# Optimization experiments

Measured on AMD Instinct MI355X. Metric: run time of the kernel, lower is better.

## Reference

```python
import jax, jax.numpy as jnp
import numpy as np

B, N, P = 8, 4096, 1024
P4 = P // 4
EPS = 1e-5


def _ln(x, g, b):
    mu = jnp.mean(x, axis=-1, keepdims=True)
    var = jnp.var(x, axis=-1, keepdims=True)
    return (x - mu) * jax.lax.rsqrt(var + EPS) * g + b


def setup_inputs() -> dict:
    key = jax.random.key(0)
    ks = jax.random.split(key, 16)
    s = lambda fan: 1.0 / np.sqrt(fan)
    return {
        "xyz": jax.random.normal(ks[0], (B, N, 3), jnp.float32),
        "x": jax.random.normal(ks[1], (B, N, P), jnp.float32),
        "ln1_g": jnp.ones((P,), jnp.float32),
        "ln1_b": jnp.zeros((P,), jnp.float32),
        "ln2_g": jnp.ones((P,), jnp.float32),
        "ln2_b": jnp.zeros((P,), jnp.float32),
        "qk_w": jax.random.normal(ks[2], (P4, P), jnp.float32) * s(P),   # shared q/k 1x1 conv, no bias
        "v_w": jax.random.normal(ks[3], (P, P), jnp.float32) * s(P),
        "v_b": jax.random.normal(ks[4], (P,), jnp.float32) * s(P),
        "t1_w": jax.random.normal(ks[5], (P, P4), jnp.float32) * s(P4),  # trans_conv
        "t1_b": jax.random.normal(ks[6], (P,), jnp.float32) * s(P4),
        "t2_w": jax.random.normal(ks[7], (P, P4), jnp.float32) * s(P4),  # trans_conv1
        "t2_b": jax.random.normal(ks[8], (P,), jnp.float32) * s(P4),
        "m1_w": jax.random.normal(ks[9], (P, P), jnp.float32) * s(P),
        "m1_b": jax.random.normal(ks[10], (P,), jnp.float32) * s(P),
        "m2_w": jax.random.normal(ks[11], (P, P), jnp.float32) * s(P),
        "m2_b": jax.random.normal(ks[12], (P,), jnp.float32) * s(P),
    }


def reference(xyz, x, ln1_g, ln1_b, ln2_g, ln2_b, qk_w, v_w, v_b,
              t1_w, t1_b, t2_w, t2_b, m1_w, m1_b, m2_w, m2_b):
    # xyz is accepted but unused, matching the torch module. Dropout = eval identity.
    res1 = x
    h = _ln(x, ln1_g, ln1_b)                                   # [B,N,P]
    # TransformerBlock_1 (1x1 convs on h^T [B,P,N] are just matmuls over P)
    x_q = jnp.einsum('op,bnp->bon', qk_w, h)                   # [B,P4,N]
    # k shares weights with q; x_k permuted is x_q transposed
    x_v = jnp.einsum('op,bnp->bno', v_w, h) + v_b              # [B,N,P]
    energy = jnp.einsum('bqn,bkn->bqk', x_q, x_q)              # [B,P4,P4]
    att = jnp.einsum('op,bpk->bok', t1_w, energy) + t1_b[:, None]   # [B,P,P4]
    att = jax.nn.gelu(att, approximate=False)
    att = jnp.einsum('op,bkp->bok', t2_w, att) + t2_b[:, None]      # [B,P,P]
    att = jax.nn.softmax(att, axis=-1)
    t_out = jnp.einsum('bnp,bpq->bnq', x_v, att)               # [B,N,P]
    x1 = t_out + res1
    h2 = _ln(x1, ln2_g, ln2_b)
    m = jax.nn.gelu(h2 @ m1_w.T + m1_b, approximate=False)
    m = m @ m2_w.T + m2_b
    return x1 + m
```

## Files before the change

### kernel.cpp

```cpp
#include <hip/hip_runtime.h>


typedef __attribute__((ext_vector_type(4))) float f32x4;
typedef __attribute__((ext_vector_type(8))) _Float16 h16x8;
typedef __attribute__((ext_vector_type(8))) unsigned short u16x8;
typedef __attribute__((ext_vector_type(4))) unsigned short u16x4;

__device__ __forceinline__ unsigned short f2h(float f) {
  _Float16 h = (_Float16)f;
  return __builtin_bit_cast(unsigned short, h);
}
__device__ __forceinline__ float h2f(unsigned short u) {
  return (float)__builtin_bit_cast(_Float16, u);
}
__device__ __forceinline__ unsigned split16(float f) {
  _Float16 h = (_Float16)f;
  _Float16 l = (_Float16)(f - (float)h);
  return (unsigned)__builtin_bit_cast(unsigned short, h) |
         ((unsigned)__builtin_bit_cast(unsigned short, l) << 16);
}
__device__ __forceinline__ float gelu_f(float x) {
  return 0.5f * x * (1.0f + erff(x * 0.70710678118654752f));
}
__device__ __forceinline__ void gload16(const void* g, void* l) {
  __builtin_amdgcn_global_load_lds(
      (const __attribute__((address_space(1))) unsigned int*)g,
      (__attribute__((address_space(3))) unsigned int*)l, 16, 0, 0);
}
#define FENCE() asm volatile("" ::: "memory")

__device__ __forceinline__ void xcd_swz(int& bx, int& by, int gx, int gy) {
  const int nwg = gx * gy;
  if ((nwg & 7) == 0 && nwg >= 16) {
    const int flat = bx + gx * by;
    const int chunk = nwg >> 3;
    const int nf = (flat & 7) * chunk + (flat >> 3);
    bx = nf % gx;
    by = nf / gx;
  }
}

__global__ __launch_bounds__(256)
void lnsplit_kernel(const float* __restrict__ x, unsigned short* __restrict__ xhi,
                    float* __restrict__ muis) {
  __shared__ float red[16];
  const size_t base = (size_t)blockIdx.x * 1024;
  const int t = threadIdx.x;
  f32x4 v = *(const f32x4*)&x[base + t * 4];
  float s = v[0] + v[1] + v[2] + v[3];
  float q = v[0] * v[0] + v[1] * v[1] + v[2] * v[2] + v[3] * v[3];
#pragma unroll
  for (int o = 32; o > 0; o >>= 1) { s += __shfl_down(s, o); q += __shfl_down(q, o); }
  const int w = t >> 6;
  if ((t & 63) == 0) { red[w] = s; red[8 + w] = q; }
  u16x4 oh;
#pragma unroll
  for (int j = 0; j < 4; j++) oh[j] = f2h(v[j]);
  *(u16x4*)&xhi[base + t * 4] = oh;
  __syncthreads();
  if (t == 0) {
    s = (red[0] + red[1]) + (red[2] + red[3]);
    q = (red[8] + red[9]) + (red[10] + red[11]);
    const float mu = s * (1.0f / 1024.0f);
    const float var = q * (1.0f / 1024.0f) - mu * mu;
    muis[blockIdx.x * 2] = mu;
    muis[blockIdx.x * 2 + 1] = rsqrtf(var + 1e-5f);
  }
}

__global__ __launch_bounds__(256)
void stats16_kernel(const unsigned short* __restrict__ x16, float* __restrict__ muis) {
  __shared__ float red[16];
  const size_t base = (size_t)blockIdx.x * 1024;
  const int t = threadIdx.x;
  u16x4 raw = *(const u16x4*)&x16[base + t * 4];
  float v[4];
#pragma unroll
  for (int j = 0; j < 4; j++) v[j] = h2f(raw[j]);
  float s = v[0] + v[1] + v[2] + v[3];
  float q = v[0] * v[0] + v[1] * v[1] + v[2] * v[2] + v[3] * v[3];
#pragma unroll
  for (int o = 32; o > 0; o >>= 1) { s += __shfl_down(s, o); q += __shfl_down(q, o); }
  const int w = t >> 6;
  if ((t & 63) == 0) { red[w] = s; red[8 + w] = q; }
  __syncthreads();
  if (t == 0) {
    s = (red[0] + red[1]) + (red[2] + red[3]);
    q = (red[8] + red[9]) + (red[10] + red[11]);
    const float mu = s * (1.0f / 1024.0f);
    const float var = q * (1.0f / 1024.0f) - mu * mu;
    muis[blockIdx.x * 2] = mu;
    muis[blockIdx.x * 2 + 1] = rsqrtf(var + 1e-5f);
  }
}

__global__ __launch_bounds__(256)
void cvt_kernel(const float* __restrict__ in, unsigned short* __restrict__ hi,
                unsigned short* __restrict__ lo, int n4) {
  int i = blockIdx.x * 256 + threadIdx.x;
  if (i < n4) {
    f32x4 v = *(const f32x4*)&in[(size_t)i * 4];
    u16x4 oh, ol;
#pragma unroll
    for (int j = 0; j < 4; j++) {
      unsigned p = split16(v[j]);
      oh[j] = (unsigned short)(p & 0xffffu);
      ol[j] = (unsigned short)(p >> 16);
    }
    *(u16x4*)&hi[(size_t)i * 4] = oh;
    if (lo) *(u16x4*)&lo[(size_t)i * 4] = ol;
  }
}

__global__ __launch_bounds__(256)
void wqprep_kernel(const float* __restrict__ qkw, const float* __restrict__ lng,
                   const float* __restrict__ lnb, unsigned short* __restrict__ wh,
                   unsigned short* __restrict__ wl, float* __restrict__ S,
                   float* __restrict__ B0) {
  __shared__ float red[16];
  const int o = blockIdx.x;
  const int t = threadIdx.x;
  const float* row = qkw + (size_t)o * 1024;
  f32x4 wv = *(const f32x4*)&row[t * 4];
  f32x4 gv = *(const f32x4*)&lng[t * 4];
  f32x4 bv = *(const f32x4*)&lnb[t * 4];
  float s = 0.0f, d = 0.0f;
  u16x4 oh, ol;
#pragma unroll
  for (int j = 0; j < 4; j++) {
    float wg = wv[j] * gv[j];
    unsigned p = split16(wg);
    oh[j] = (unsigned short)(p & 0xffffu);
    ol[j] = (unsigned short)(p >> 16);
    s += wg;
    d += wv[j] * bv[j];
  }
  *(u16x4*)&wh[(size_t)o * 1024 + t * 4] = oh;
  *(u16x4*)&wl[(size_t)o * 1024 + t * 4] = ol;
#pragma unroll
  for (int off = 32; off > 0; off >>= 1) { s += __shfl_down(s, off); d += __shfl_down(d, off); }
  const int w = t >> 6;
  if ((t & 63) == 0) { red[w] = s; red[8 + w] = d; }
  __syncthreads();
  if (t == 0) {
    S[o] = (red[0] + red[1]) + (red[2] + red[3]);
    B0[o] = (red[8] + red[9]) + (red[10] + red[11]);
  }
}

__global__ __launch_bounds__(256)
void m1prep_kernel(const float* __restrict__ m1w, const float* __restrict__ lng,
                   const float* __restrict__ lnb, const float* __restrict__ m1b,
                   unsigned short* __restrict__ wp, float* __restrict__ S,
                   float* __restrict__ b2) {
  __shared__ float red[16];
  const int o = blockIdx.x;
  const int t = threadIdx.x;
  const float* row = m1w + (size_t)o * 1024;
  f32x4 wv = *(const f32x4*)&row[t * 4];
  f32x4 gv = *(const f32x4*)&lng[t * 4];
  f32x4 bv = *(const f32x4*)&lnb[t * 4];
  float s = 0.0f, d = 0.0f;
  u16x4 ow;
#pragma unroll
  for (int j = 0; j < 4; j++) {
    float wpj = wv[j] * gv[j];
    ow[j] = f2h(wpj);
    s += wpj;
    d += wv[j] * bv[j];
  }
  *(u16x4*)&wp[(size_t)o * 1024 + t * 4] = ow;
#pragma unroll
  for (int off = 32; off > 0; off >>= 1) { s += __shfl_down(s, off); d += __shfl_down(d, off); }
  const int w = t >> 6;
  if ((t & 63) == 0) { red[w] = s; red[8 + w] = d; }
  __syncthreads();
  if (t == 0) {
    S[o] = (red[0] + red[1]) + (red[2] + red[3]);
    b2[o] = m1b[o] + (red[8] + red[9]) + (red[10] + red[11]);
  }
}

__global__ __launch_bounds__(256)
void vwvec_kernel(const float* __restrict__ vw, const float* __restrict__ lng,
                  const float* __restrict__ lnb, const float* __restrict__ vb,
                  float* __restrict__ gv, float* __restrict__ vb2) {
  __shared__ float red[16];
  const int p = blockIdx.x;
  const int t = threadIdx.x;
  const float* row = vw + (size_t)p * 1024;
  f32x4 wv = *(const f32x4*)&row[t * 4];
  f32x4 gg = *(const f32x4*)&lng[t * 4];
  f32x4 bb = *(const f32x4*)&lnb[t * 4];
  float s = 0.0f, d = 0.0f;
#pragma unroll
  for (int j = 0; j < 4; j++) { s += wv[j] * gg[j]; d += wv[j] * bb[j]; }
#pragma unroll
  for (int off = 32; off > 0; off >>= 1) { s += __shfl_down(s, off); d += __shfl_down(d, off); }
  const int w = t >> 6;
  if ((t & 63) == 0) { red[w] = s; red[8 + w] = d; }
  __syncthreads();
  if (t == 0) {
    gv[p] = (red[0] + red[1]) + (red[2] + red[3]);
    vb2[p] = vb[p] + (red[8] + red[9]) + (red[10] + red[11]);
  }
}

__global__ __launch_bounds__(256)
void vwt_kernel(const float* __restrict__ vw, const float* __restrict__ lng,
                unsigned short* __restrict__ wvt) {
  __shared__ float T[64][65];
  const int bx = blockIdx.x, by = blockIdx.y;
  const int t = threadIdx.x;
  const int lr = t >> 6, lc = t & 63;
#pragma unroll
  for (int i = 0; i < 16; ++i) {
    const int row = i * 4 + lr;
    T[row][lc] = vw[(size_t)(by * 64 + row) * 1024 + bx * 64 + lc];
  }
  __syncthreads();
#pragma unroll
  for (int i = 0; i < 16; ++i) {
    const int row = i * 4 + lr;
    wvt[(size_t)(bx * 64 + row) * 1024 + by * 64 + lc] =
        f2h(T[lc][row] * lng[bx * 64 + row]);
  }
}

__global__ __launch_bounds__(256)
void attdots_kernel(const unsigned short* __restrict__ attT, const float* __restrict__ vb2,
                    const float* __restrict__ gv, float* __restrict__ add1,
                    float* __restrict__ Sg) {
  const int b = blockIdx.y;
  const int q = blockIdx.x * 4 + (threadIdx.x >> 6);
  const int l = threadIdx.x & 63;
  const unsigned short* row = attT + ((size_t)b * 1024 + q) * 1024;
  float s = 0.0f, d = 0.0f;
#pragma unroll
  for (int i = 0; i < 2; ++i) {
    u16x8 v = *(const u16x8*)&row[(i * 64 + l) * 8];
#pragma unroll
    for (int j = 0; j < 8; j++) {
      const float a = h2f(v[j]);
      const int idx = (i * 64 + l) * 8 + j;
      s += a * vb2[idx];
      d += a * gv[idx];
    }
  }
#pragma unroll
  for (int o = 32; o > 0; o >>= 1) { s += __shfl_down(s, o); d += __shfl_down(d, o); }
  if (l == 0) { add1[b * 1024 + q] = s; Sg[b * 1024 + q] = d; }
}

template <int EPI>
__global__ __launch_bounds__(256)
void gemm_v(const unsigned short* __restrict__ Ain, const unsigned short* __restrict__ Bin,
            void* __restrict__ Cout, const float* __restrict__ bias,
            const unsigned short* __restrict__ res16In, const float* __restrict__ muis,
            const float* __restrict__ Svec,
            int K, int lda, int ldb, int ldc,
            long long sA, long long sB, long long sC, long long sBias, long long sRes) {
  __shared__ short As[2][4096];
  __shared__ short Bs[2][4096];
  const int z = blockIdx.z;
  const unsigned short* A = Ain + (size_t)z * sA;
  const unsigned short* B = Bin + (size_t)z * sB;
  int bx = blockIdx.x, by = blockIdx.y;
  xcd_swz(bx, by, gridDim.x, gridDim.y);
  const int mBase = by * 128, nBase = bx * 128;
  const int t = threadIdx.x, w = t >> 6, l = t & 63;
  const int r16 = l & 15, kq = l >> 4;
  const int wr = (w >> 1) * 64, wc = (w & 1) * 64;
  f32x4 acc[4][4] = {};

  auto stage = [&](int buf, int k0) {
#pragma unroll
    for (int i = 0; i < 2; ++i) {
      const int c = i * 256 + t;
      const int row = c >> 2, cc = c & 3;
      const int gc = cc ^ ((row >> 1) & 3);
      short* la = &As[buf][(i * 256 + w * 64) * 8];
      short* lb = &Bs[buf][(i * 256 + w * 64) * 8];
      gload16(&A[(size_t)(mBase + row) * lda + k0 + gc * 8], la);
      gload16(&B[(size_t)(nBase + row) * ldb + k0 + gc * 8], lb);
    }
  };

  const int nt = K >> 5;
  stage(0, 0);
  if (nt > 1) stage(1, 32);
  for (int ts = 0; ts < nt; ++ts) {
    const int cur = ts & 1;
    if (ts + 1 < nt) { asm volatile("s_waitcnt vmcnt(4)" ::: "memory"); }
    else             { asm volatile("s_waitcnt vmcnt(0)" ::: "memory"); }
    __builtin_amdgcn_s_barrier();
    FENCE();
    h16x8 aF[4], bF[4];
#pragma unroll
    for (int mi = 0; mi < 4; mi++) {
      const int r = wr + mi * 16 + r16;
      aF[mi] = *(const h16x8*)&As[cur][r * 32 + (kq ^ ((r >> 1) & 3)) * 8];
    }
#pragma unroll
    for (int ni = 0; ni < 4; ni++) {
      const int r = wc + ni * 16 + r16;
      bF[ni] = *(const h16x8*)&Bs[cur][r * 32 + (kq ^ ((r >> 1) & 3)) * 8];
    }
    __builtin_amdgcn_s_setprio(1);
#pragma unroll
    for (int mi = 0; mi < 4; mi++)
#pragma unroll
      for (int ni = 0; ni < 4; ni++)
        acc[mi][ni] = __builtin_amdgcn_mfma_f32_16x16x32_f16(aF[mi], bF[ni], acc[mi][ni], 0, 0, 0);
    __builtin_amdgcn_s_setprio(0);
    FENCE();
    __builtin_amdgcn_s_barrier();
    FENCE();
    if (ts + 2 < nt) stage(cur, (ts + 2) * 32);
  }
  FENCE();

  unsigned short* C16 = (unsigned short*)Cout + (size_t)z * sC;
  float* C32 = (float*)Cout + (size_t)z * sC;
  const float* bp = (EPI != 4) ? bias + (size_t)z * sBias : nullptr;
  const unsigned short* rp = (EPI == 3) ? res16In + (size_t)z * sRes : nullptr;

  if constexpr (EPI == 4 || EPI == 9) {
    short* ep = ((w & 2) ? &Bs[0][0] : &As[0][0]) + (w & 1) * 4096;
#pragma unroll
    for (int mi = 0; mi < 4; mi++) {
      float mu[4], is[4];
      if (EPI == 9) {
#pragma unroll
        for (int r = 0; r < 4; r++) {
          const int rw = mBase + wr + mi * 16 + kq * 4 + r;
          mu[r] = muis[rw * 2];
          is[r] = muis[rw * 2 + 1];
        }
      }
#pragma unroll
      for (int ni = 0; ni < 4; ni++) {
        const int cl = nBase + wc + ni * 16 + r16;
        const float bcol = bp ? bp[cl] : 0.0f;
        const float Scol = (EPI == 9) ? Svec[cl] : 0.0f;
#pragma unroll
        for (int r = 0; r < 4; r++) {
          float v;
          if (EPI == 9) v = gelu_f(is[r] * (acc[mi][ni][r] - mu[r] * Scol) + bcol);
          else          v = acc[mi][ni][r] + bcol;
          ep[(mi * 16 + kq * 4 + r) * 64 + ni * 16 + r16] = (short)f2h(v);
        }
      }
    }
#pragma unroll
    for (int j = 0; j < 8; j++) {
      const int f = j * 512 + l * 8;
      const int row = f >> 6, col = f & 63;
      const size_t gi = (size_t)(mBase + wr + row) * ldc + nBase + wc + col;
      *(u16x8*)&C16[gi] = *(const u16x8*)&ep[f];
    }
  } else {
#pragma unroll
    for (int mi = 0; mi < 4; mi++) {
#pragma unroll
      for (int ni = 0; ni < 4; ni++) {
        const int cl = nBase + wc + ni * 16 + r16;
        const float bcol = bp[cl];
#pragma unroll
        for (int r = 0; r < 4; r++) {
          const int rw = mBase + wr + mi * 16 + kq * 4 + r;
          const size_t idx = (size_t)rw * ldc + cl;
          C32[idx] = acc[mi][ni][r] + bcol + h2f(rp[idx]);
        }
      }
    }
  }
}

__global__ __launch_bounds__(256)
void gemm_r(const unsigned short* __restrict__ Ain, const unsigned short* __restrict__ Bin,
            unsigned short* __restrict__ Cout, const float* __restrict__ muis,
            const float* __restrict__ SgIn, const float* __restrict__ add1In,
            const unsigned short* __restrict__ resIn,
            int K, int lda, int ldb, int ldc,
            long long sA, long long sB, long long sC, long long sRes) {
  __shared__ short As[2][4096];
  __shared__ short Bs[2][4096];
  const int z = blockIdx.z;
  const unsigned short* A = Ain + (size_t)z * sA;
  const unsigned short* B = Bin + (size_t)z * sB;
  int bx = blockIdx.x, by = blockIdx.y;
  xcd_swz(bx, by, gridDim.x, gridDim.y);
  const int mBase = by * 128, nBase = bx * 128;
  const int t = threadIdx.x, w = t >> 6, l = t & 63;
  const int r16 = l & 15, kq = l >> 4;
  const int wr = (w >> 1) * 64, wc = (w & 1) * 64;
  f32x4 acc[4][4] = {};

  const int row0 = t >> 2, row1 = 64 + (t >> 2);
  const int cc0 = t & 3;
  const int gc0 = cc0 ^ ((row0 >> 1) & 3);
  const int gc1 = cc0 ^ ((row1 >> 1) & 3);

  u16x8 ra0, ra1, rb0, rb1;
  auto loadreg = [&](int k0) {
    ra0 = *(const u16x8*)&A[(size_t)(mBase + row0) * lda + k0 + gc0 * 8];
    rb0 = *(const u16x8*)&B[(size_t)(nBase + row0) * ldb + k0 + gc0 * 8];
    ra1 = *(const u16x8*)&A[(size_t)(mBase + row1) * lda + k0 + gc1 * 8];
    rb1 = *(const u16x8*)&B[(size_t)(nBase + row1) * ldb + k0 + gc1 * 8];
  };
  auto dswrite = [&](int buf) {
    *(u16x8*)&As[buf][t * 8] = ra0;
    *(u16x8*)&Bs[buf][t * 8] = rb0;
    *(u16x8*)&As[buf][(256 + t) * 8] = ra1;
    *(u16x8*)&Bs[buf][(256 + t) * 8] = rb1;
  };

  const int nt = K >> 5;
  loadreg(0);
  dswrite(0);
  if (nt > 1) loadreg(32);
  asm volatile("s_waitcnt lgkmcnt(0)" ::: "memory");
  __builtin_amdgcn_s_barrier();
  FENCE();
  for (int ts = 0; ts < nt; ++ts) {
    const int cur = ts & 1;
    h16x8 aF[4], bF[4];
#pragma unroll
    for (int mi = 0; mi < 4; mi++) {
      const int r = wr + mi * 16 + r16;
      aF[mi] = *(const h16x8*)&As[cur][r * 32 + (kq ^ ((r >> 1) & 3)) * 8];
    }
#pragma unroll
    for (int ni = 0; ni < 4; ni++) {
      const int r = wc + ni * 16 + r16;
      bF[ni] = *(const h16x8*)&Bs[cur][r * 32 + (kq ^ ((r >> 1) & 3)) * 8];
    }
    __builtin_amdgcn_s_setprio(1);
#pragma unroll
    for (int mi = 0; mi < 4; mi++)
#pragma unroll
      for (int ni = 0; ni < 4; ni++)
        acc[mi][ni] = __builtin_amdgcn_mfma_f32_16x16x32_f16(aF[mi], bF[ni], acc[mi][ni], 0, 0, 0);
    __builtin_amdgcn_s_setprio(0);
    FENCE();
    if (ts + 1 < nt) {
      __builtin_amdgcn_s_barrier();
      FENCE();
      dswrite((ts + 1) & 1);
      if (ts + 2 < nt) loadreg((ts + 2) * 32);
      asm volatile("s_waitcnt lgkmcnt(0)" ::: "memory");
      FENCE();
      __builtin_amdgcn_s_barrier();
      FENCE();
    }
  }
  FENCE();

  unsigned short* C16 = Cout + (size_t)z * sC;
  const float* muz = muis + (size_t)z * 8192;
  const float* Sg = SgIn + (size_t)z * 1024;
  const float* ad = add1In + (size_t)z * 1024;
  const unsigned short* rp = resIn + (size_t)z * sRes;
  short* ep = ((w & 2) ? &Bs[0][0] : &As[0][0]) + (w & 1) * 4096;
#pragma unroll
  for (int mi = 0; mi < 4; mi++) {
    float mu[4], is[4];
#pragma unroll
    for (int r = 0; r < 4; r++) {
      const int rw = mBase + wr + mi * 16 + kq * 4 + r;
      mu[r] = muz[rw * 2];
      is[r] = muz[rw * 2 + 1];
    }
#pragma unroll
    for (int ni = 0; ni < 4; ni++) {
      const int cl = nBase + wc + ni * 16 + r16;
      const float sgc = Sg[cl];
      const float adc = ad[cl];
#pragma unroll
      for (int r = 0; r < 4; r++)
        ep[(mi * 16 + kq * 4 + r) * 64 + ni * 16 + r16] =
            (short)f2h(is[r] * (acc[mi][ni][r] - mu[r] * sgc) + adc);
    }
  }
#pragma unroll
  for (int j = 0; j < 8; j++) {
    const int f = j * 512 + l * 8;
    const int row = f >> 6, col = f & 63;
    u16x8 v8 = *(const u16x8*)&ep[f];
    const size_t gi = (size_t)(mBase + wr + row) * ldc + nBase + wc + col;
    u16x8 r8 = *(const u16x8*)&rp[gi];
#pragma unroll
    for (int q = 0; q < 8; q++) v8[q] = f2h(h2f(v8[q]) + h2f(r8[q]));
    *(u16x8*)&C16[gi] = v8;
  }
}

__global__ __launch_bounds__(256)
void gemm_q(const unsigned short* __restrict__ Ahi, const unsigned short* __restrict__ Alo,
            const float* __restrict__ Bf32,
            unsigned short* __restrict__ Cout, unsigned short* __restrict__ Cout2,
            const float* __restrict__ Svec, const float* __restrict__ B0vec,
            const float* __restrict__ mu1,
            int K, int lda, int ldb, int ldc,
            long long sB, long long sC) {
  __shared__ short As[2][8192];
  __shared__ float Bs[2][4096];
  const int z = blockIdx.z;
  const float* B = Bf32 + (size_t)z * sB;
  int bx = blockIdx.x, by = blockIdx.y;
  xcd_swz(bx, by, gridDim.x, gridDim.y);
  const int mBase = bx * 128, nBase = by * 128;
  const int t = threadIdx.x, w = t >> 6, l = t & 63;
  const int r16 = l & 15, kq = l >> 4;
  const int wr = (w >> 1) * 64, wc = (w & 1) * 64;
  f32x4 acc[4][4] = {};

  auto stage = [&](int buf, int k0) {
#pragma unroll
    for (int i = 0; i < 2; ++i) {
      const int c = i * 256 + t;
      const int row = c >> 2, cc = c & 3;
      const int gc = cc ^ ((row >> 1) & 3);
      const int cbase = i * 256 + w * 64;
      const size_t ga = (size_t)(mBase + row) * lda + k0 + gc * 8;
      gload16(&Ahi[ga], &As[buf][cbase * 8]);
      gload16(&Alo[ga], &As[buf][4096 + cbase * 8]);
    }
#pragma unroll
    for (int i = 0; i < 4; ++i) {
      const int c = i * 256 + t;
      const int row = c >> 3, cc = c & 7;
      const int gc = cc ^ (row & 7);
      const int cbase = i * 256 + w * 64;
      gload16(&B[(size_t)(nBase + row) * ldb + k0 + gc * 4], &Bs[buf][cbase * 4]);
    }
  };

  const int nsteps = K >> 5;
  stage(0, 0);
  if (nsteps > 1) stage(1, 32);
  for (int ts = 0; ts < nsteps; ++ts) {
    const int cur = ts & 1;
    if (ts + 1 < nsteps) { asm volatile("s_waitcnt vmcnt(8)" ::: "memory"); }
    else                 { asm volatile("s_waitcnt vmcnt(0)" ::: "memory"); }
    __builtin_amdgcn_s_barrier();
    FENCE();
    h16x8 aH[4], bH[4], aL[4], bL[4];
#pragma unroll
    for (int mi = 0; mi < 4; mi++) {
      const int r = wr + mi * 16 + r16;
      const int off = r * 32 + (kq ^ ((r >> 1) & 3)) * 8;
      aH[mi] = *(const h16x8*)&As[cur][off];
      aL[mi] = *(const h16x8*)&As[cur][4096 + off];
    }
#pragma unroll
    for (int ni = 0; ni < 4; ni++) {
      const int r = wc + ni * 16 + r16;
      const int swz = r & 7;
      f32x4 v0 = *(const f32x4*)&Bs[cur][r * 32 + ((2 * kq) ^ swz) * 4];
      f32x4 v1 = *(const f32x4*)&Bs[cur][r * 32 + ((2 * kq + 1) ^ swz) * 4];
#pragma unroll
      for (int j = 0; j < 4; j++) {
        _Float16 h0 = (_Float16)v0[j];
        _Float16 h1 = (_Float16)v1[j];
        bH[ni][j] = h0;       bH[ni][j + 4] = h1;
        bL[ni][j] = (_Float16)(v0[j] - (float)h0);
        bL[ni][j + 4] = (_Float16)(v1[j] - (float)h1);
      }
    }
    __builtin_amdgcn_s_setprio(1);
#pragma unroll
    for (int mi = 0; mi < 4; mi++)
#pragma unroll
      for (int ni = 0; ni < 4; ni++) {
        acc[mi][ni] = __builtin_amdgcn_mfma_f32_16x16x32_f16(aH[mi], bH[ni], acc[mi][ni], 0, 0, 0);
        acc[mi][ni] = __builtin_amdgcn_mfma_f32_16x16x32_f16(aH[mi], bL[ni], acc[mi][ni], 0, 0, 0);
        acc[mi][ni] = __builtin_amdgcn_mfma_f32_16x16x32_f16(aL[mi], bH[ni], acc[mi][ni], 0, 0, 0);
      }
    __builtin_amdgcn_s_setprio(0);
    FENCE();
    __builtin_amdgcn_s_barrier();
    FENCE();
    if (ts + 2 < nsteps) stage(cur, (ts + 2) * 32);
  }
  FENCE();

  unsigned short* C16 = Cout + (size_t)z * sC;
  unsigned short* C16b = Cout2 + (size_t)z * sC;
  const float* mu1b = mu1 + (size_t)z * 8192;
  short* ep = &As[0][0] + w * 4096;
  unsigned pk[4][4][4];
#pragma unroll
  for (int mi = 0; mi < 4; mi++)
#pragma unroll
    for (int ni = 0; ni < 4; ni++) {
      const int cl = nBase + wc + ni * 16 + r16;
      const float muc = mu1b[cl * 2];
      const float isc = mu1b[cl * 2 + 1];
#pragma unroll
      for (int r = 0; r < 4; r++) {
        const int rw = mBase + wr + mi * 16 + kq * 4 + r;
        float v = isc * (acc[mi][ni][r] - muc * Svec[rw]) + B0vec[rw];
        pk[mi][ni][r] = split16(v);
      }
    }
#pragma unroll
  for (int mi = 0; mi < 4; mi++)
#pragma unroll
    for (int ni = 0; ni < 4; ni++)
#pragma unroll
      for (int r = 0; r < 4; r++)
        ep[(mi * 16 + kq * 4 + r) * 64 + ni * 16 + r16] =
            (short)(pk[mi][ni][r] & 0xffffu);
#pragma unroll
  for (int j = 0; j < 8; j++) {
    const int f = j * 512 + l * 8;
    const int row = f >> 6, col = f & 63;
    *(u16x8*)&C16[(size_t)(mBase + wr + row) * ldc + nBase + wc + col] =
        *(const u16x8*)&ep[f];
  }
#pragma unroll
  for (int mi = 0; mi < 4; mi++)
#pragma unroll
    for (int ni = 0; ni < 4; ni++)
#pragma unroll
      for (int r = 0; r < 4; r++)
        ep[(mi * 16 + kq * 4 + r) * 64 + ni * 16 + r16] =
            (short)(pk[mi][ni][r] >> 16);
#pragma unroll
  for (int j = 0; j < 8; j++) {
    const int f = j * 512 + l * 8;
    const int row = f >> 6, col = f & 63;
    *(u16x8*)&C16b[(size_t)(mBase + wr + row) * ldc + nBase + wc + col] =
        *(const u16x8*)&ep[f];
  }
}

template <int EPI>
__global__ __launch_bounds__(256)
void gemm_s(const unsigned short* __restrict__ Ahi, const unsigned short* __restrict__ Alo,
            const unsigned short* __restrict__ Bhi, const unsigned short* __restrict__ Blo,
            void* __restrict__ Cout, unsigned short* __restrict__ Cout2,
            const float* __restrict__ bias,
            int K, int lda, int ldb, int ldc,
            long long sA, long long sB, long long sC, int splitK) {
  __shared__ short As[2][8192];
  __shared__ short Bs[2][8192];
  const int z = blockIdx.z;
  const int bi = z / splitK, sp = z % splitK;
  const int kLen = K / splitK, kStart = sp * kLen;
  const unsigned short* AH = Ahi + (size_t)bi * sA;
  const unsigned short* BH = Bhi + (size_t)bi * sB;
  const unsigned short* AL = Alo + (size_t)bi * sA;
  const unsigned short* BL = Blo + (size_t)bi * sB;
  int bx = blockIdx.x, by = blockIdx.y;
  xcd_swz(bx, by, gridDim.x, gridDim.y);
  const int mBase = by * 128, nBase = bx * 128;
  const int t = threadIdx.x, w = t >> 6, l = t & 63;
  const int r16 = l & 15, kq = l >> 4;
  const int wr = (w >> 1) * 64, wc = (w & 1) * 64;
  f32x4 acc[4][4] = {};

  auto stage = [&](int buf, int k0) {
#pragma unroll
    for (int i = 0; i < 2; ++i) {
      const int c = i * 256 + t;
      const int row = c >> 2, cc = c & 3;
      const int gc = cc ^ ((row >> 1) & 3);
      const int cbase = i * 256 + w * 64;
      const size_t ga = (size_t)(mBase + row) * lda + k0 + gc * 8;
      const size_t gb = (size_t)(nBase + row) * ldb + k0 + gc * 8;
      gload16(&AH[ga], &As[buf][cbase * 8]);
      gload16(&AL[ga], &As[buf][4096 + cbase * 8]);
      gload16(&BH[gb], &Bs[buf][cbase * 8]);
      gload16(&BL[gb], &Bs[buf][4096 + cbase * 8]);
    }
  };

  const int nsteps = kLen >> 5;
  stage(0, kStart);
  if (nsteps > 1) stage(1, kStart + 32);
  for (int ts = 0; ts < nsteps; ++ts) {
    const int cur = ts & 1;
    if (ts + 1 < nsteps) { asm volatile("s_waitcnt vmcnt(8)" ::: "memory"); }
    else                 { asm volatile("s_waitcnt vmcnt(0)" ::: "memory"); }
    __builtin_amdgcn_s_barrier();
    FENCE();
    h16x8 aH[4], bH[4], aL[4], bL[4];
#pragma unroll
    for (int mi = 0; mi < 4; mi++) {
      const int r = wr + mi * 16 + r16;
      const int off = r * 32 + (kq ^ ((r >> 1) & 3)) * 8;
      aH[mi] = *(const h16x8*)&As[cur][off];
      aL[mi] = *(const h16x8*)&As[cur][4096 + off];
    }
#pragma unroll
    for (int ni = 0; ni < 4; ni++) {
      const int r = wc + ni * 16 + r16;
      const int off = r * 32 + (kq ^ ((r >> 1) & 3)) * 8;
      bH[ni] = *(const h16x8*)&Bs[cur][off];
      bL[ni] = *(const h16x8*)&Bs[cur][4096 + off];
    }
    __builtin_amdgcn_s_setprio(1);
#pragma unroll
    for (int mi = 0; mi < 4; mi++)
#pragma unroll
      for (int ni = 0; ni < 4; ni++) {
        acc[mi][ni] = __builtin_amdgcn_mfma_f32_16x16x32_f16(aH[mi], bH[ni], acc[mi][ni], 0, 0, 0);
        acc[mi][ni] = __builtin_amdgcn_mfma_f32_16x16x32_f16(aH[mi], bL[ni], acc[mi][ni], 0, 0, 0);
        acc[mi][ni] = __builtin_amdgcn_mfma_f32_16x16x32_f16(aL[mi], bH[ni], acc[mi][ni], 0, 0, 0);
      }
    __builtin_amdgcn_s_setprio(0);
    FENCE();
    __builtin_amdgcn_s_barrier();
    FENCE();
    if (ts + 2 < nsteps) stage(cur, kStart + (ts + 2) * 32);
  }
  FENCE();

  unsigned short* C16 = (unsigned short*)Cout + (size_t)z * sC;
  unsigned short* C16b = Cout2 ? Cout2 + (size_t)z * sC : nullptr;
  float* C32 = (float*)Cout + (size_t)z * sC;

  if constexpr (EPI == 6) {
    short* ep = &As[0][0] + w * 4096;
    unsigned pk[4][4][4];
#pragma unroll
    for (int mi = 0; mi < 4; mi++)
#pragma unroll
      for (int ni = 0; ni < 4; ni++)
#pragma unroll
        for (int r = 0; r < 4; r++) {
          float v = acc[mi][ni][r] + bias[mBase + wr + mi * 16 + kq * 4 + r];
          pk[mi][ni][r] = split16(gelu_f(v));
        }
#pragma unroll
    for (int mi = 0; mi < 4; mi++)
#pragma unroll
      for (int ni = 0; ni < 4; ni++)
#pragma unroll
        for (int r = 0; r < 4; r++)
          ep[(mi * 16 + kq * 4 + r) * 64 + ni * 16 + r16] =
              (short)(pk[mi][ni][r] & 0xffffu);
#pragma unroll
    for (int j = 0; j < 8; j++) {
      const int f = j * 512 + l * 8;
      const int row = f >> 6, col = f & 63;
      *(u16x8*)&C16[(size_t)(mBase + wr + row) * ldc + nBase + wc + col] =
          *(const u16x8*)&ep[f];
    }
#pragma unroll
    for (int mi = 0; mi < 4; mi++)
#pragma unroll
      for (int ni = 0; ni < 4; ni++)
#pragma unroll
        for (int r = 0; r < 4; r++)
          ep[(mi * 16 + kq * 4 + r) * 64 + ni * 16 + r16] =
              (short)(pk[mi][ni][r] >> 16);
#pragma unroll
    for (int j = 0; j < 8; j++) {
      const int f = j * 512 + l * 8;
      const int row = f >> 6, col = f & 63;
      *(u16x8*)&C16b[(size_t)(mBase + wr + row) * ldc + nBase + wc + col] =
          *(const u16x8*)&ep[f];
    }
  } else {
#pragma unroll
    for (int mi = 0; mi < 4; mi++) {
#pragma unroll
      for (int ni = 0; ni < 4; ni++) {
        const int cl = nBase + wc + ni * 16 + r16;
#pragma unroll
        for (int r = 0; r < 4; r++) {
          const int rw = mBase + wr + mi * 16 + kq * 4 + r;
          float v = acc[mi][ni][r];
          if (EPI == 7) v += bias[rw];
          C32[(size_t)rw * ldc + cl] = v;
        }
      }
    }
  }
}

__global__ __launch_bounds__(256)
void ereduce_kernel(const float* __restrict__ part, unsigned short* __restrict__ ehi,
                    unsigned short* __restrict__ elo) {
  const size_t idx = (size_t)blockIdx.x * 256 + threadIdx.x;
  const size_t b = idx >> 16, i = idx & 65535;
  const float* p = part + b * (8ull * 65536) + i;
  float s0 = (p[0] + p[65536]) + (p[2 * 65536] + p[3 * 65536]);
  float s1 = (p[4 * 65536] + p[5 * 65536]) + (p[6 * 65536] + p[7 * 65536]);
  unsigned pk = split16(s0 + s1);
  ehi[idx] = (unsigned short)(pk & 0xffffu);
  elo[idx] = (unsigned short)(pk >> 16);
}

__global__ __launch_bounds__(256)
void smax_t_kernel(const float* __restrict__ a2, unsigned short* __restrict__ attT) {
  __shared__ float S[8][1028];
  __shared__ float inv[8];
  const int t = threadIdx.x;
  const int b = blockIdx.y;
  const int o0 = blockIdx.x * 8;
  const float* src = a2 + ((size_t)b * 1024 + o0) * 1024;
#pragma unroll
  for (int i = 0; i < 8; i++)
    *(f32x4*)&S[i][t * 4] = *(const f32x4*)&src[(size_t)i * 1024 + t * 4];
  __syncthreads();
  const int w = t >> 6, l = t & 63;
  for (int rr = 0; rr < 2; rr++) {
    const int r = w * 2 + rr;
    float m = -1e30f;
#pragma unroll
    for (int i = 0; i < 16; i++) m = fmaxf(m, S[r][l + i * 64]);
#pragma unroll
    for (int o = 32; o > 0; o >>= 1) m = fmaxf(m, __shfl_xor(m, o));
    float ssum = 0.0f;
#pragma unroll
    for (int i = 0; i < 16; i++) {
      float e = expf(S[r][l + i * 64] - m);
      S[r][l + i * 64] = e;
      ssum += e;
    }
#pragma unroll
    for (int o = 32; o > 0; o >>= 1) ssum += __shfl_xor(ssum, o);
    if (l == 0) inv[r] = 1.0f / ssum;
  }
  __syncthreads();
  float iv[8];
#pragma unroll
  for (int r = 0; r < 8; r++) iv[r] = inv[r];
#pragma unroll
  for (int i = 0; i < 4; i++) {
    const int k = i * 256 + t;
    u16x8 ov;
#pragma unroll
    for (int r = 0; r < 8; r++) ov[r] = f2h(S[r][k] * iv[r]);
    *(u16x8*)&attT[((size_t)b * 1024 + k) * 1024 + o0] = ov;
  }
}

extern "C" void kernel_launch(void* const* d_in, const int* in_sizes, int n_in,
                              void* d_out, int out_size, void* d_ws, size_t ws_size,
                              hipStream_t stream) {
  (void)in_sizes; (void)n_in; (void)out_size; (void)ws_size;
  const float* x     = (const float*)d_in[1];
  const float* ln1_g = (const float*)d_in[2];
  const float* ln1_b = (const float*)d_in[3];
  const float* ln2_g = (const float*)d_in[4];
  const float* ln2_b = (const float*)d_in[5];
  const float* qk_w  = (const float*)d_in[6];
  const float* v_w   = (const float*)d_in[7];
  const float* v_b   = (const float*)d_in[8];
  const float* t1_w  = (const float*)d_in[9];
  const float* t1_b  = (const float*)d_in[10];
  const float* t2_w  = (const float*)d_in[11];
  const float* t2_b  = (const float*)d_in[12];
  const float* m1_w  = (const float*)d_in[13];
  const float* m1_b  = (const float*)d_in[14];
  const float* m2_w  = (const float*)d_in[15];
  const float* m2_b  = (const float*)d_in[16];

  char* ws = (char*)d_ws;
  unsigned short* xhi  = (unsigned short*)(ws + 0);
  unsigned short* gb   = (unsigned short*)(ws + 67108864);
  unsigned short* Qthi = (unsigned short*)(ws + 134217728);
  unsigned short* Qtlo = (unsigned short*)(ws + 150994944);
  float*          part = (float*)(ws + 167772160);
  unsigned short* Ehi  = (unsigned short*)(ws + 184549376);
  unsigned short* Elo  = (unsigned short*)(ws + 185597952);
  unsigned short* Ghi  = (unsigned short*)(ws + 186646528);
  unsigned short* Glo  = (unsigned short*)(ws + 190840832);
  float*          a2   = (float*)(ws + 195035136);
  unsigned short* attT = (unsigned short*)(ws + 228589568);
  unsigned short* WeT  = (unsigned short*)(ws + 245366784);
  float*          add1 = (float*)(ws + 262144000);
  float*          Sg   = (float*)(ws + 262176768);
  float*          muis1= (float*)(ws + 262209536);
  float*          muis2= (float*)(ws + 262471680);
  float*          SvM1 = (float*)(ws + 262733824);
  float*          b2   = (float*)(ws + 262737920);
  float*          SQt  = (float*)(ws + 262742016);
  float*          B0Qt = (float*)(ws + 262746112);
  float*          gv   = (float*)(ws + 262750208);
  float*          vb2  = (float*)(ws + 262754304);
  unsigned short* x1h  = (unsigned short*)(ws + 335544320);
  unsigned short* wqh  = (unsigned short*)(ws + 446693376);
  unsigned short* wql  = (unsigned short*)(ws + 447217664);
  unsigned short* wvt  = (unsigned short*)(ws + 447741952);
  unsigned short* wt1h = (unsigned short*)(ws + 449839104);
  unsigned short* wt1l = (unsigned short*)(ws + 450363392);
  unsigned short* wt2h = (unsigned short*)(ws + 450887680);
  unsigned short* wt2l = (unsigned short*)(ws + 451411968);
  unsigned short* wm1p = (unsigned short*)(ws + 451936256);
  unsigned short* wm2  = (unsigned short*)(ws + 454033408);
  float* out = (float*)d_out;

  wqprep_kernel<<<dim3(256), dim3(256), 0, stream>>>(qk_w, ln1_g, ln1_b, wqh, wql, SQt, B0Qt);
  vwt_kernel<<<dim3(16, 16), dim3(256), 0, stream>>>(v_w, ln1_g, wvt);
  vwvec_kernel<<<dim3(1024), dim3(256), 0, stream>>>(v_w, ln1_g, ln1_b, v_b, gv, vb2);
  cvt_kernel<<<dim3(256),  dim3(256), 0, stream>>>(t1_w, wt1h, wt1l, 65536);
  cvt_kernel<<<dim3(256),  dim3(256), 0, stream>>>(t2_w, wt2h, wt2l, 65536);
  m1prep_kernel<<<dim3(1024), dim3(256), 0, stream>>>(m1_w, ln2_g, ln2_b, m1_b, wm1p, SvM1, b2);
  cvt_kernel<<<dim3(1024), dim3(256), 0, stream>>>(m2_w, wm2, nullptr, 262144);
  lnsplit_kernel<<<dim3(32768), dim3(256), 0, stream>>>(x, xhi, muis1);
  gemm_q<<<dim3(2, 32, 8), dim3(256), 0, stream>>>(
      wqh, wql, x, Qthi, Qtlo, SQt, B0Qt, muis1,
      1024, 1024, 1024, 4096, 4194304, 1048576);
  gemm_s<5><<<dim3(2, 2, 64), dim3(256), 0, stream>>>(
      Qthi, Qtlo, Qthi, Qtlo, part, nullptr, nullptr,
      4096, 4096, 4096, 256, 1048576, 1048576, 65536, 8);
  ereduce_kernel<<<dim3(2048), dim3(256), 0, stream>>>(part, Ehi, Elo);
  gemm_s<6><<<dim3(2, 8, 8), dim3(256), 0, stream>>>(
      wt1h, wt1l, Ehi, Elo, Ghi, Glo, t1_b,
      256, 256, 256, 256, 0, 65536, 262144, 1);
  gemm_s<7><<<dim3(8, 8, 8), dim3(256), 0, stream>>>(
      wt2h, wt2l, Ghi, Glo, a2, nullptr, t2_b,
      256, 256, 256, 1024, 0, 262144, 1048576, 1);
  smax_t_kernel<<<dim3(128, 8), dim3(256), 0, stream>>>(a2, attT);
  gemm_v<4><<<dim3(8, 8, 8), dim3(256), 0, stream>>>(
      attT, wvt, WeT, nullptr, nullptr, nullptr, nullptr,
      1024, 1024, 1024, 1024, 1048576, 0, 1048576, 0, 0);
  attdots_kernel<<<dim3(256, 8), dim3(256), 0, stream>>>(attT, vb2, gv, add1, Sg);
  gemm_r<<<dim3(8, 32, 8), dim3(256), 0, stream>>>(
      xhi, WeT, x1h, muis1, Sg, add1, xhi,
      1024, 1024, 1024, 1024, 4194304, 1048576, 4194304, 4194304);
  stats16_kernel<<<dim3(32768), dim3(256), 0, stream>>>(x1h, muis2);
  gemm_v<9><<<dim3(8, 256, 1), dim3(256), 0, stream>>>(
      x1h, wm1p, gb, b2, nullptr, muis2, SvM1,
      1024, 1024, 1024, 1024, 0, 0, 0, 0, 0);
  gemm_v<3><<<dim3(8, 256, 1), dim3(256), 0, stream>>>(
      gb, wm2, out, m2_b, x1h, nullptr, nullptr,
      1024, 1024, 1024, 1024, 0, 0, 0, 0, 0);
}
```

Measured before the change: 625.0 us.

## Use 256x256-tile 8-wave pipelined GEMM for the two MLP matmuls

Adds a new gemm_p kernel with 256x256 output tiles, 512 threads, 128-wide K steps and double-buffered LDS loaded in half-tile stages interleaved with MFMA phases. It replaces the generic 128x128 gemm_v for the MLP GELU (EPI 9) and residual (EPI 3) GEMMs, which are the large 32768x1024x1024 matmuls. The larger tiles raise arithmetic intensity and reduce global traffic, at the cost of one block per CU (launch_bounds 512,1), more registers and 128KB of LDS. The gemm_v epilogue is trimmed to only the plain store path that remains in use.

```diff
diff --git a/kernel.cpp b/kernel.cpp
--- a/kernel.cpp
+++ b/kernel.cpp
@@ -250,6 +250,168 @@
 #pragma unroll
   for (int o = 32; o > 0; o >>= 1) { s += __shfl_down(s, o); d += __shfl_down(d, o); }
   if (l == 0) { add1[b * 1024 + q] = s; Sg[b * 1024 + q] = d; }
+}
+
+template <int EPI>
+__global__ __launch_bounds__(512, 1)
+void gemm_p(const unsigned short* __restrict__ Ain, const unsigned short* __restrict__ Bin,
+            void* __restrict__ Cout, const float* __restrict__ bias,
+            const unsigned short* __restrict__ res16In, const float* __restrict__ muis,
+            const float* __restrict__ Svec,
+            int K, int lda, int ldb, int ldc) {
+  __shared__ short As[2][16384];
+  __shared__ short Bs[2][16384];
+  int bx = blockIdx.x, by = blockIdx.y;
+  xcd_swz(bx, by, gridDim.x, gridDim.y);
+  const int mBase = by * 256, nBase = bx * 256;
+  const int t = threadIdx.x, w = t >> 6, l = t & 63;
+  const int r16 = l & 15, kq = l >> 4;
+  const int wr = (w >> 2) * 128, wc = (w & 3) * 64;
+  f32x4 acc[8][4] = {};
+
+  auto stage_half = [&](int buf, int mat, int h, int k0) {
+#pragma unroll
+    for (int i = 0; i < 2; ++i) {
+      const int c = i * 512 + t;
+      const int row = c >> 3, cc = c & 7;
+      const int gc = cc ^ (row & 7);
+      const int cbase = i * 512 + w * 64;
+      if (mat == 0)
+        gload16(&Ain[(size_t)(mBase + h * 128 + row) * lda + k0 + gc * 8],
+                &As[buf][(h * 1024 + cbase) * 8]);
+      else
+        gload16(&Bin[(size_t)(nBase + h * 128 + row) * ldb + k0 + gc * 8],
+                &Bs[buf][(h * 1024 + cbase) * 8]);
+    }
+  };
+
+  const int NT2 = K >> 7;
+  stage_half(0, 0, 0, 0);
+  stage_half(0, 0, 1, 0);
+  stage_half(0, 1, 0, 0);
+  stage_half(0, 1, 1, 0);
+
+  for (int it = 0; it < NT2; ++it) {
+#pragma unroll
+    for (int p = 0; p < 8; ++p) {
+      const int kt = p >> 2;
+      const int buf = kt;
+      const int q = p & 3;
+      const int mih = q >> 1, nih = q & 1;
+      const bool haveStage = (p < 4) ? true : (it + 1 < NT2);
+      const int skt = (p < 4) ? (2 * it + 1) : (2 * it + 2);
+      const int sbuf = skt & 1;
+      const int smat = q >> 1, sh = q & 1;
+
+      h16x8 aF[4][2], bF[2][2];
+      if (p == 0 || p == 4) {
+        if (haveStage) {
+          stage_half(sbuf, smat, sh, skt * 64);
+          asm volatile("s_waitcnt vmcnt(2)" ::: "memory");
+        } else {
+          asm volatile("s_waitcnt vmcnt(0)" ::: "memory");
+        }
+        __builtin_amdgcn_s_barrier();
+        FENCE();
+#pragma unroll
+        for (int mi = 0; mi < 4; mi++) {
+          const int r = wr + (mih * 4 + mi) * 16 + r16;
+#pragma unroll
+          for (int kk = 0; kk < 2; kk++)
+            aF[mi][kk] = *(const h16x8*)&As[buf][r * 64 + ((kk * 4 + kq) ^ (r & 7)) * 8];
+        }
+#pragma unroll
+        for (int ni = 0; ni < 2; ni++) {
+          const int r = wc + (nih * 2 + ni) * 16 + r16;
+#pragma unroll
+          for (int kk = 0; kk < 2; kk++)
+            bF[ni][kk] = *(const h16x8*)&Bs[buf][r * 64 + ((kk * 4 + kq) ^ (r & 7)) * 8];
+        }
+      } else {
+#pragma unroll
+        for (int mi = 0; mi < 4; mi++) {
+          const int r = wr + (mih * 4 + mi) * 16 + r16;
+#pragma unroll
+          for (int kk = 0; kk < 2; kk++)
+            aF[mi][kk] = *(const h16x8*)&As[buf][r * 64 + ((kk * 4 + kq) ^ (r & 7)) * 8];
+        }
+#pragma unroll
+        for (int ni = 0; ni < 2; ni++) {
+          const int r = wc + (nih * 2 + ni) * 16 + r16;
+#pragma unroll
+          for (int kk = 0; kk < 2; kk++)
+            bF[ni][kk] = *(const h16x8*)&Bs[buf][r * 64 + ((kk * 4 + kq) ^ (r & 7)) * 8];
+        }
+        if (haveStage) stage_half(sbuf, smat, sh, skt * 64);
+        FENCE();
+        __builtin_amdgcn_s_barrier();
+        FENCE();
+      }
+      __builtin_amdgcn_s_setprio(1);
+#pragma unroll
+      for (int mi = 0; mi < 4; mi++)
+#pragma unroll
+        for (int ni = 0; ni < 2; ni++)
+#pragma unroll
+          for (int kk = 0; kk < 2; kk++)
+            acc[mih * 4 + mi][nih * 2 + ni] = __builtin_amdgcn_mfma_f32_16x16x32_f16(
+                aF[mi][kk], bF[ni][kk], acc[mih * 4 + mi][nih * 2 + ni], 0, 0, 0);
+      __builtin_amdgcn_s_setprio(0);
+      FENCE();
+      __builtin_amdgcn_s_barrier();
+      FENCE();
+    }
+  }
+  FENCE();
+
+  unsigned short* C16 = (unsigned short*)Cout;
+  float* C32 = (float*)Cout;
+  if constexpr (EPI == 9) {
+    short* ep = (w < 4 ? &As[0][0] : &Bs[0][0]) + (w & 3) * 8192;
+#pragma unroll
+    for (int mi = 0; mi < 8; mi++) {
+      float mu[4], is[4];
+#pragma unroll
+      for (int r = 0; r < 4; r++) {
+        const int rw = mBase + wr + mi * 16 + kq * 4 + r;
+        mu[r] = muis[rw * 2];
+        is[r] = muis[rw * 2 + 1];
+      }
+#pragma unroll
+      for (int ni = 0; ni < 4; ni++) {
+        const int cl = nBase + wc + ni * 16 + r16;
+        const float bcol = bias[cl];
+        const float Scol = Svec[cl];
+#pragma unroll
+        for (int r = 0; r < 4; r++) {
+          float v = gelu_f(is[r] * (acc[mi][ni][r] - mu[r] * Scol) + bcol);
+          ep[(mi * 16 + kq * 4 + r) * 64 + ni * 16 + r16] = (short)f2h(v);
+        }
+      }
+    }
+#pragma unroll
+    for (int j = 0; j < 16; j++) {
+      const int f = j * 512 + l * 8;
+      const int row = f >> 6, col = f & 63;
+      const size_t gi = (size_t)(mBase + wr + row) * ldc + nBase + wc + col;
+      *(u16x8*)&C16[gi] = *(const u16x8*)&ep[f];
+    }
+  } else {
+#pragma unroll
+    for (int mi = 0; mi < 8; mi++) {
+#pragma unroll
+      for (int ni = 0; ni < 4; ni++) {
+        const int cl = nBase + wc + ni * 16 + r16;
+        const float bcol = bias[cl];
+#pragma unroll
+        for (int r = 0; r < 4; r++) {
+          const int rw = mBase + wr + mi * 16 + kq * 4 + r;
+          const size_t idx = (size_t)rw * ldc + cl;
+          C32[idx] = acc[mi][ni][r] + bcol + h2f(res16In[idx]);
+        }
+      }
+    }
+  }
 }
 
 template <int EPI>
@@ -321,59 +483,22 @@
   FENCE();
 
   unsigned short* C16 = (unsigned short*)Cout + (size_t)z * sC;
-  float* C32 = (float*)Cout + (size_t)z * sC;
-  const float* bp = (EPI != 4) ? bias + (size_t)z * sBias : nullptr;
-  const unsigned short* rp = (EPI == 3) ? res16In + (size_t)z * sRes : nullptr;
-
-  if constexpr (EPI == 4 || EPI == 9) {
-    short* ep = ((w & 2) ? &Bs[0][0] : &As[0][0]) + (w & 1) * 4096;
-#pragma unroll
-    for (int mi = 0; mi < 4; mi++) {
-      float mu[4], is[4];
-      if (EPI == 9) {
-#pragma unroll
-        for (int r = 0; r < 4; r++) {
-          const int rw = mBase + wr + mi * 16 + kq * 4 + r;
-          mu[r] = muis[rw * 2];
-          is[r] = muis[rw * 2 + 1];
-        }
-      }
-#pragma unroll
-      for (int ni = 0; ni < 4; ni++) {
-        const int cl = nBase + wc + ni * 16 + r16;
-        const float bcol = bp ? bp[cl] : 0.0f;
-        const float Scol = (EPI == 9) ? Svec[cl] : 0.0f;
-#pragma unroll
-        for (int r = 0; r < 4; r++) {
-          float v;
-          if (EPI == 9) v = gelu_f(is[r] * (acc[mi][ni][r] - mu[r] * Scol) + bcol);
-          else          v = acc[mi][ni][r] + bcol;
-          ep[(mi * 16 + kq * 4 + r) * 64 + ni * 16 + r16] = (short)f2h(v);
-        }
-      }
-    }
-#pragma unroll
-    for (int j = 0; j < 8; j++) {
-      const int f = j * 512 + l * 8;
-      const int row = f >> 6, col = f & 63;
-      const size_t gi = (size_t)(mBase + wr + row) * ldc + nBase + wc + col;
-      *(u16x8*)&C16[gi] = *(const u16x8*)&ep[f];
-    }
-  } else {
-#pragma unroll
-    for (int mi = 0; mi < 4; mi++) {
-#pragma unroll
-      for (int ni = 0; ni < 4; ni++) {
-        const int cl = nBase + wc + ni * 16 + r16;
-        const float bcol = bp[cl];
-#pragma unroll
-        for (int r = 0; r < 4; r++) {
-          const int rw = mBase + wr + mi * 16 + kq * 4 + r;
-          const size_t idx = (size_t)rw * ldc + cl;
-          C32[idx] = acc[mi][ni][r] + bcol + h2f(rp[idx]);
-        }
-      }
-    }
+  short* ep = ((w & 2) ? &Bs[0][0] : &As[0][0]) + (w & 1) * 4096;
+#pragma unroll
+  for (int mi = 0; mi < 4; mi++) {
+#pragma unroll
+    for (int ni = 0; ni < 4; ni++) {
+#pragma unroll
+      for (int r = 0; r < 4; r++)
+        ep[(mi * 16 + kq * 4 + r) * 64 + ni * 16 + r16] = (short)f2h(acc[mi][ni][r]);
+    }
+  }
+#pragma unroll
+  for (int j = 0; j < 8; j++) {
+    const int f = j * 512 + l * 8;
+    const int row = f >> 6, col = f & 63;
+    const size_t gi = (size_t)(mBase + wr + row) * ldc + nBase + wc + col;
+    *(u16x8*)&C16[gi] = *(const u16x8*)&ep[f];
   }
 }
 
@@ -927,10 +1052,8 @@
       xhi, WeT, x1h, muis1, Sg, add1, xhi,
       1024, 1024, 1024, 1024, 4194304, 1048576, 4194304, 4194304);
   stats16_kernel<<<dim3(32768), dim3(256), 0, stream>>>(x1h, muis2);
-  gemm_v<9><<<dim3(8, 256, 1), dim3(256), 0, stream>>>(
-      x1h, wm1p, gb, b2, nullptr, muis2, SvM1,
-      1024, 1024, 1024, 1024, 0, 0, 0, 0, 0);
-  gemm_v<3><<<dim3(8, 256, 1), dim3(256), 0, stream>>>(
-      gb, wm2, out, m2_b, x1h, nullptr, nullptr,
-      1024, 1024, 1024, 1024, 0, 0, 0, 0, 0);
-}
+  gemm_p<9><<<dim3(4, 128, 1), dim3(512), 0, stream>>>(
+      x1h, wm1p, gb, b2, nullptr, muis2, SvM1, 1024, 1024, 1024, 1024);
+  gemm_p<3><<<dim3(4, 128, 1), dim3(512), 0, stream>>>(
+      gb, wm2, out, m2_b, x1h, nullptr, nullptr, 1024, 1024, 1024, 1024);
+}
```

Measured after the change: 634.3 us. No clear change (+1.5%).
